# Optimization experiments

Measured on AMD Instinct MI355X. Metric: run time of the kernel, lower is better.

Reference implementation:

```python
import jax, jax.numpy as jnp
import numpy as np

GRID_SIZE = 5
SPLINE_ORDER = 3
GRID_MIN = -1.0
GRID_MAX = 1.0
H = (GRID_MAX - GRID_MIN) / GRID_SIZE          # grid interval
G0 = GRID_MIN - SPLINE_ORDER * H               # first (extended) knot = grid[:,0]


def _basis_matrix():
    # Uniform B-spline power-basis matrix, same recurrence as the torch code.
    M = np.array([[1.0]], dtype=np.float64)
    scalar = 1.0
    for k in range(2, SPLINE_ORDER + 2):
        t1 = np.pad(M, ((0, 1), (0, 0)))
        t3 = np.pad(M, ((1, 0), (0, 0)))
        t2 = np.zeros((k - 1, k))
        t4 = np.zeros((k - 1, k))
        for i in range(k - 1):
            t2[i, i] = i + 1
            t2[i, i + 1] = k - (i + 2)
            t4[i, i] = -1.0
            t4[i, i + 1] = 1.0
        M = t1 @ t2 + t3 @ t4
        scalar *= 1.0 / (k - 1)
    return (M * scalar).astype(np.float32)

BASIS = jnp.asarray(_basis_matrix())  # (spline_order+1, spline_order+1)


def setup_inputs():
    key = jax.random.key(0)
    k1, k2, k3 = jax.random.split(key, 3)
    N, FIN, FOUT = 2048, 128, 128
    x = jax.random.normal(k1, (N, FIN), dtype=jnp.float32)
    base_weight = jax.random.normal(k2, (FOUT, FIN), dtype=jnp.float32) * 0.1
    spline_weight = jax.random.normal(k3, (FIN, FOUT, GRID_SIZE + SPLINE_ORDER), dtype=jnp.float32) * 0.1
    return {"x": x, "base_weight": base_weight, "spline_weight": spline_weight}


def _forward(x, base_weight, spline_weight):
    N, fin = x.shape
    fout = base_weight.shape[0]
    k = SPLINE_ORDER
    # base branch: SiLU activation then linear
    base_out = jax.nn.silu(x) @ base_weight.T                       # (N, fout)
    # input normalization: Hardtanh around grid center (shift=0, scale=1 for [-1,1])
    shift = (GRID_MIN + GRID_MAX) / 2.0
    scale = (GRID_MAX - GRID_MIN) / 2.0
    xn = jnp.clip((x - shift) / scale, -1.0, 1.0) * scale + shift
    # bucketize: bin index + fractional position (replaces floor/compare + torch.nonzero)
    t = (xn - G0) / H
    fl = jnp.floor(t)
    u1 = t - fl                                                     # (x - interval_floor) / interval
    idx = jnp.clip(fl.astype(jnp.int32), k, k + GRID_SIZE - 1)      # clamped knot-interval index
    cfloor = idx - k                                                # (N, fin) first control point index
    # power bases [1, u, u^2, ..., u^k] -> b-spline basis via basis matrix
    pows = u1[..., None] ** jnp.arange(k + 1, dtype=x.dtype)        # (N, fin, k+1)
    bspl = pows @ BASIS.astype(x.dtype)                             # (N, fin, k+1)
    # faithful to torch: spline_weight.view(out, in, -1) memory reinterpretation
    cp = jnp.reshape(spline_weight, (fout, fin, GRID_SIZE + k))
    gidx = cfloor[..., None] + jnp.arange(k + 1)                    # (N, fin, k+1) control point indices
    i_idx = jnp.arange(fin)[None, :, None]
    gathered = cp[:, i_idx, gidx]                                   # (fout, N, fin, k+1)
    gathered = jnp.transpose(gathered, (1, 0, 2, 3))                # (N, fout, fin, k+1)
    # faithful to torch: .view(N, in, k+1, out) memory reinterpretation
    cpr = jnp.reshape(gathered, (N, fin, k + 1, fout))
    # per-feature spline matmul then sum over in_features (KAN aggregation)
    spline_out = jnp.einsum('nij,nijo->no', bspl, cpr)              # (N, fout)
    return base_out + spline_out


def reference(x, base_weight, spline_weight):
    return _forward(x, base_weight, spline_weight)
```

## Files before the change

kernel.cpp:

```cpp
#include <hip/hip_runtime.h>
#include <hip/hip_bf16.h>
#include <math.h>

typedef __attribute__((ext_vector_type(8))) short short8;
typedef __attribute__((ext_vector_type(4))) float floatx4;

static __device__ __forceinline__ unsigned short bfbits(float f) {
    __hip_bfloat16 h = __float2bfloat16(f);
    unsigned short u;
    __builtin_memcpy(&u, &h, 2);
    return u;
}
static __device__ __forceinline__ unsigned pack2(float lo, float hi) {
    return (unsigned)bfbits(lo) | ((unsigned)bfbits(hi) << 16);
}

__global__ __launch_bounds__(256) void kan_prep(
    const float* __restrict__ bw, const float* __restrict__ sw,
    unsigned char* __restrict__ ws)
{
    __shared__ float buf[128 * 65];
    __hip_bfloat16* Bt = (__hip_bfloat16*)ws;
    const int blk = blockIdx.x;
    const int tid = threadIdx.x;

    if (blk < 16) {
        const int a  = tid >> 1;
        const int jh = (tid & 1) * 32;
        const float* src = sw + a * 1024 + blk * 64 + jh;
        float* dst = buf + a * 65 + jh;
#pragma unroll
        for (int i = 0; i < 32; ++i) dst[i] = src[i];
        __syncthreads();
        const int jl = tid >> 2;
        const int aq = (tid & 3) * 32;
        unsigned p[16];
#pragma unroll
        for (int i = 0; i < 16; ++i)
            p[i] = pack2(buf[(aq + 2*i) * 65 + jl], buf[(aq + 2*i + 1) * 65 + jl]);
        uint4* o = (uint4*)(Bt + (blk * 64 + jl) * 128 + aq);
        o[0] = make_uint4(p[0], p[1], p[2], p[3]);
        o[1] = make_uint4(p[4], p[5], p[6], p[7]);
        o[2] = make_uint4(p[8], p[9], p[10], p[11]);
        o[3] = make_uint4(p[12], p[13], p[14], p[15]);
    } else {
        int base = (blk - 16) * 8192 + tid * 32;
        unsigned p[16];
#pragma unroll
        for (int i = 0; i < 8; ++i) {
            float4 v = *(const float4*)(bw + base + i * 4);
            p[2*i]     = pack2(v.x, v.y);
            p[2*i + 1] = pack2(v.z, v.w);
        }
        uint4* o = (uint4*)(Bt + 1024 * 128 + base);
#pragma unroll
        for (int i = 0; i < 4; ++i)
            o[i] = make_uint4(p[4*i], p[4*i+1], p[4*i+2], p[4*i+3]);
    }
}

#define SB_STR 136
#define SP_STR 136
#define ST_STR 68
#define SC_STR 132

__global__ __launch_bounds__(256) void kan_main(
    const float* __restrict__ x,
    const unsigned char* __restrict__ ws,
    float* __restrict__ out)
{
    __shared__ __hip_bfloat16 sP[5 * 16 * SP_STR];
    __shared__ __hip_bfloat16 sB[2][64 * SB_STR];
    __shared__ float sT[2][16 * ST_STR];
    __shared__ unsigned char sC[16 * SC_STR];

    const __hip_bfloat16* Bt = (const __hip_bfloat16*)ws;
    const int tid = threadIdx.x;
    const int nb  = blockIdx.x >> 2;
    const int s   = blockIdx.x & 3;
    const int n0  = nb * 16;

    {
        const int r  = tid >> 4;
        const int i0 = (tid & 15) * 8;
        float v[8];
        *(float4*)(v)     = *(const float4*)(x + (n0 + r) * 128 + i0);
        *(float4*)(v + 4) = *(const float4*)(x + (n0 + r) * 128 + i0 + 4);
        float A5[5][8];
        unsigned char cc8[8];
#pragma unroll
        for (int i = 0; i < 8; ++i) {
            float xv = v[i];
            float si = xv / (1.0f + expf(-xv));
            float xn = fminf(fmaxf(xv, -1.0f), 1.0f);
            float t  = (xn + 2.2f) / 0.4f;
            float u  = t - floorf(t);
            int idx  = (int)floorf(t);
            idx = min(max(idx, 3), 7);
            cc8[i] = (unsigned char)(idx - 3);
            float u2 = u * u, u3 = u2 * u, om = 1.0f - u;
            A5[0][i] = om * om * om * (1.0f / 6.0f);
            A5[1][i] = 0.5f * u3 - u2 + (2.0f / 3.0f);
            A5[2][i] = -0.5f * u3 + 0.5f * u2 + 0.5f * u + (1.0f / 6.0f);
            A5[3][i] = u3 * (1.0f / 6.0f);
            A5[4][i] = si;
        }
#pragma unroll
        for (int g = 0; g < 5; ++g) {
            unsigned p0 = pack2(A5[g][0], A5[g][1]);
            unsigned p1 = pack2(A5[g][2], A5[g][3]);
            unsigned p2 = pack2(A5[g][4], A5[g][5]);
            unsigned p3 = pack2(A5[g][6], A5[g][7]);
            *(uint4*)(sP + (g * 16 + r) * SP_STR + i0) = make_uint4(p0, p1, p2, p3);
        }
        *(unsigned*)(sC + r * SC_STR + i0)     = cc8[0] | (cc8[1]<<8) | (cc8[2]<<16) | (cc8[3]<<24);
        *(unsigned*)(sC + r * SC_STR + i0 + 4) = cc8[4] | (cc8[5]<<8) | (cc8[6]<<16) | (cc8[7]<<24);
    }

    const int w = tid >> 6, l = tid & 63;
    const int m = l & 15, q = l >> 4;
    const int gn  = tid >> 4;
    const int go2 = tid & 15;
    const int br   = tid >> 2;
    const int bseg = (tid & 3) * 32;

    float racc0 = 0.f, racc1 = 0.f;

    uint4 breg[4];
    {
        const uint4* src = (const uint4*)(Bt + (s * 64 + br) * 128 + bseg);
#pragma unroll
        for (int i = 0; i < 4; ++i) breg[i] = src[i];
    }

    for (int t = 0; t < 5; ++t) {
        const int p = t & 1;
        if (t < 4 || tid < 128) {
#pragma unroll
            for (int i = 0; i < 4; ++i)
                *(uint4*)(&sB[p][br * SB_STR + bseg + i * 8]) = breg[i];
        }
        __syncthreads();

        if (t < 3) {
            const uint4* src = (const uint4*)(Bt + ((s + 4*(t+1)) * 64 + br) * 128 + bseg);
#pragma unroll
            for (int i = 0; i < 4; ++i) breg[i] = src[i];
        } else if (t == 3) {
            if (tid < 128) {
                const uint4* src = (const uint4*)(Bt + (1024 + s * 32 + br) * 128 + bseg);
#pragma unroll
                for (int i = 0; i < 4; ++i) breg[i] = src[i];
            }
        }

        if (t > 0) {
            const int tb = t - 1;
            if (tb < 4) {
                int oh  = 8 * s + (go2 >> 1);
                int c   = sC[gn * SC_STR + 32 * tb + oh];
                int rel = 8 * (go2 >> 1) + c + 2 * (go2 & 1);
                racc0 += sT[1 - p][gn * ST_STR + rel];
                racc1 += sT[1 - p][gn * ST_STR + rel + 1];
            }
        }

        if (t < 4 || w < 2) {
            floatx4 acc = {0.f, 0.f, 0.f, 0.f};
#pragma unroll
            for (int kk = 0; kk < 4; ++kk) {
                short8 af  = *(const short8*)(sP + (t * 16 + m) * SP_STR + q * 8 + kk * 32);
                short8 bfr = *(const short8*)(&sB[p][(16 * w + m) * SB_STR + q * 8 + kk * 32]);
                acc = __builtin_amdgcn_mfma_f32_16x16x32_bf16(af, bfr, acc, 0, 0, 0);
            }
#pragma unroll
            for (int r = 0; r < 4; ++r)
                sT[p][(q * 4 + r) * ST_STR + 16 * w + m] = acc[r];
        }
    }
    __syncthreads();
    racc0 += sT[0][gn * ST_STR + 2 * go2];
    racc1 += sT[0][gn * ST_STR + 2 * go2 + 1];

    float2 o2 = make_float2(racc0, racc1);
    *(float2*)(out + (n0 + gn) * 128 + 32 * s + 2 * go2) = o2;
}

extern "C" void kernel_launch(void* const* d_in, const int* in_sizes, int n_in,
                              void* d_out, int out_size, void* d_ws, size_t ws_size,
                              hipStream_t stream) {
    const float* x  = (const float*)d_in[0];
    const float* bw = (const float*)d_in[1];
    const float* sw = (const float*)d_in[2];
    float* out = (float*)d_out;
    unsigned char* ws = (unsigned char*)d_ws;
    kan_prep<<<dim3(18),  dim3(256), 0, stream>>>(bw, sw, ws);
    kan_main<<<dim3(512), dim3(256), 0, stream>>>(x, ws, out);
}
```

Before: 71.26 us.

## Fuse weight prep into main kernel, converting fp32 weights to bf16 per block

Removes the separate prep kernel that transposed and converted spline and base weights to bf16 in a workspace. Each main block now loads fp32 weight slices directly, packs them to bf16 in registers and stores them untransposed in shared memory. The MFMA B fragments are then gathered with strided scalar LDS reads. This saves one kernel launch and the serial dependency between the two kernels, but every block redoes the conversion and reads twice as many weight bytes, and the strided B reads are costlier.

```diff
diff --git a/kernel.cpp b/kernel.cpp
--- a/kernel.cpp
+++ b/kernel.cpp
@@ -15,77 +15,44 @@
     return (unsigned)bfbits(lo) | ((unsigned)bfbits(hi) << 16);
 }
 
-__global__ __launch_bounds__(256) void kan_prep(
-    const float* __restrict__ bw, const float* __restrict__ sw,
-    unsigned char* __restrict__ ws)
-{
-    __shared__ float buf[128 * 65];
-    __hip_bfloat16* Bt = (__hip_bfloat16*)ws;
-    const int blk = blockIdx.x;
-    const int tid = threadIdx.x;
+#define SP_STR  136
+#define SBN_STR 76
+#define SBB_STR 136
+#define ST_STR  68
+#define SC_STR  132
 
-    if (blk < 16) {
-        const int a  = tid >> 1;
-        const int jh = (tid & 1) * 32;
-        const float* src = sw + a * 1024 + blk * 64 + jh;
-        float* dst = buf + a * 65 + jh;
-#pragma unroll
-        for (int i = 0; i < 32; ++i) dst[i] = src[i];
-        __syncthreads();
-        const int jl = tid >> 2;
-        const int aq = (tid & 3) * 32;
-        unsigned p[16];
-#pragma unroll
-        for (int i = 0; i < 16; ++i)
-            p[i] = pack2(buf[(aq + 2*i) * 65 + jl], buf[(aq + 2*i + 1) * 65 + jl]);
-        uint4* o = (uint4*)(Bt + (blk * 64 + jl) * 128 + aq);
-        o[0] = make_uint4(p[0], p[1], p[2], p[3]);
-        o[1] = make_uint4(p[4], p[5], p[6], p[7]);
-        o[2] = make_uint4(p[8], p[9], p[10], p[11]);
-        o[3] = make_uint4(p[12], p[13], p[14], p[15]);
-    } else {
-        int base = (blk - 16) * 8192 + tid * 32;
-        unsigned p[16];
-#pragma unroll
-        for (int i = 0; i < 8; ++i) {
-            float4 v = *(const float4*)(bw + base + i * 4);
-            p[2*i]     = pack2(v.x, v.y);
-            p[2*i + 1] = pack2(v.z, v.w);
-        }
-        uint4* o = (uint4*)(Bt + 1024 * 128 + base);
-#pragma unroll
-        for (int i = 0; i < 4; ++i)
-            o[i] = make_uint4(p[4*i], p[4*i+1], p[4*i+2], p[4*i+3]);
-    }
-}
-
-#define SB_STR 136
-#define SP_STR 136
-#define ST_STR 68
-#define SC_STR 132
-
-__global__ __launch_bounds__(256) void kan_main(
+__global__ __launch_bounds__(256) void kan_fused(
     const float* __restrict__ x,
-    const unsigned char* __restrict__ ws,
+    const float* __restrict__ bw,
+    const float* __restrict__ sw,
     float* __restrict__ out)
 {
-    __shared__ __hip_bfloat16 sP[5 * 16 * SP_STR];
-    __shared__ __hip_bfloat16 sB[2][64 * SB_STR];
+    __shared__ short sP[5 * 16 * SP_STR];
+    __shared__ short sBn[2][128 * SBN_STR];
+    __shared__ short sBb[32 * SBB_STR];
     __shared__ float sT[2][16 * ST_STR];
     __shared__ unsigned char sC[16 * SC_STR];
 
-    const __hip_bfloat16* Bt = (const __hip_bfloat16*)ws;
     const int tid = threadIdx.x;
     const int nb  = blockIdx.x >> 2;
     const int s   = blockIdx.x & 3;
     const int n0  = nb * 16;
 
+    const int ar = tid >> 4;
+    const int sg = tid & 15;
+
+    const int r  = tid >> 4;
+    const int i0 = (tid & 15) * 8;
+    float v[8];
+    *(float4*)(v)     = *(const float4*)(x + (n0 + r) * 128 + i0);
+    *(float4*)(v + 4) = *(const float4*)(x + (n0 + r) * 128 + i0 + 4);
+
+    float4 pre[8];
+#pragma unroll
+    for (int rr = 0; rr < 8; ++rr)
+        pre[rr] = *(const float4*)(sw + (ar + 16 * rr) * 1024 + s * 64 + sg * 4);
+
     {
-        const int r  = tid >> 4;
-        const int i0 = (tid & 15) * 8;
-        float v[8];
-        *(float4*)(v)     = *(const float4*)(x + (n0 + r) * 128 + i0);
-        *(float4*)(v + 4) = *(const float4*)(x + (n0 + r) * 128 + i0 + 4);
         float A5[5][8];
         unsigned char cc8[8];
 #pragma unroll
@@ -111,79 +78,108 @@
             unsigned p1 = pack2(A5[g][2], A5[g][3]);
             unsigned p2 = pack2(A5[g][4], A5[g][5]);
             unsigned p3 = pack2(A5[g][6], A5[g][7]);
-            *(uint4*)(sP + (g * 16 + r) * SP_STR + i0) = make_uint4(p0, p1, p2, p3);
+            *(uint4*)(&sP[(g * 16 + r) * SP_STR + i0]) = make_uint4(p0, p1, p2, p3);
         }
-        *(unsigned*)(sC + r * SC_STR + i0)     = cc8[0] | (cc8[1]<<8) | (cc8[2]<<16) | (cc8[3]<<24);
-        *(unsigned*)(sC + r * SC_STR + i0 + 4) = cc8[4] | (cc8[5]<<8) | (cc8[6]<<16) | (cc8[7]<<24);
+        *(unsigned*)(&sC[r * SC_STR + i0])     = cc8[0] | (cc8[1]<<8) | (cc8[2]<<16) | (cc8[3]<<24);
+        *(unsigned*)(&sC[r * SC_STR + i0 + 4]) = cc8[4] | (cc8[5]<<8) | (cc8[6]<<16) | (cc8[7]<<24);
     }
 
     const int w = tid >> 6, l = tid & 63;
     const int m = l & 15, q = l >> 4;
     const int gn  = tid >> 4;
     const int go2 = tid & 15;
-    const int br   = tid >> 2;
-    const int bseg = (tid & 3) * 32;
+
+    uint2 pk[8];
+#pragma unroll
+    for (int rr = 0; rr < 8; ++rr)
+        pk[rr] = make_uint2(pack2(pre[rr].x, pre[rr].y), pack2(pre[rr].z, pre[rr].w));
 
     float racc0 = 0.f, racc1 = 0.f;
+    float4 bpre[4];
 
-    uint4 breg[4];
-    {
-        const uint4* src = (const uint4*)(Bt + (s * 64 + br) * 128 + bseg);
 #pragma unroll
-        for (int i = 0; i < 4; ++i) breg[i] = src[i];
-    }
-
-    for (int t = 0; t < 5; ++t) {
+    for (int t = 0; t < 4; ++t) {
         const int p = t & 1;
-        if (t < 4 || tid < 128) {
 #pragma unroll
-            for (int i = 0; i < 4; ++i)
-                *(uint4*)(&sB[p][br * SB_STR + bseg + i * 8]) = breg[i];
-        }
+        for (int rr = 0; rr < 8; ++rr)
+            *(uint2*)(&sBn[p][(ar + 16 * rr) * SBN_STR + sg * 4]) = pk[rr];
         __syncthreads();
 
         if (t < 3) {
-            const uint4* src = (const uint4*)(Bt + ((s + 4*(t+1)) * 64 + br) * 128 + bseg);
 #pragma unroll
-            for (int i = 0; i < 4; ++i) breg[i] = src[i];
-        } else if (t == 3) {
-            if (tid < 128) {
-                const uint4* src = (const uint4*)(Bt + (1024 + s * 32 + br) * 128 + bseg);
+            for (int rr = 0; rr < 8; ++rr)
+                pre[rr] = *(const float4*)(sw + (ar + 16 * rr) * 1024 + (s + 4 * (t + 1)) * 64 + sg * 4);
+        } else {
 #pragma unroll
-                for (int i = 0; i < 4; ++i) breg[i] = src[i];
+            for (int i = 0; i < 4; ++i) {
+                int e = i * 256 + tid;
+                bpre[i] = *(const float4*)(bw + (32 * s + (e >> 5)) * 128 + (e & 31) * 4);
             }
         }
 
         if (t > 0) {
-            const int tb = t - 1;
-            if (tb < 4) {
-                int oh  = 8 * s + (go2 >> 1);
-                int c   = sC[gn * SC_STR + 32 * tb + oh];
-                int rel = 8 * (go2 >> 1) + c + 2 * (go2 & 1);
-                racc0 += sT[1 - p][gn * ST_STR + rel];
-                racc1 += sT[1 - p][gn * ST_STR + rel + 1];
-            }
+            int oh  = 8 * s + (go2 >> 1);
+            int c   = sC[gn * SC_STR + 32 * (t - 1) + oh];
+            int rel = 8 * (go2 >> 1) + c + 2 * (go2 & 1);
+            racc0 += sT[1 - p][gn * ST_STR + rel];
+            racc1 += sT[1 - p][gn * ST_STR + rel + 1];
         }
 
-        if (t < 4 || w < 2) {
-            floatx4 acc = {0.f, 0.f, 0.f, 0.f};
+        floatx4 acc = {0.f, 0.f, 0.f, 0.f};
 #pragma unroll
-            for (int kk = 0; kk < 4; ++kk) {
-                short8 af  = *(const short8*)(sP + (t * 16 + m) * SP_STR + q * 8 + kk * 32);
-                short8 bfr = *(const short8*)(&sB[p][(16 * w + m) * SB_STR + q * 8 + kk * 32]);
-                acc = __builtin_amdgcn_mfma_f32_16x16x32_bf16(af, bfr, acc, 0, 0, 0);
-            }
+        for (int kk = 0; kk < 4; ++kk) {
+            short8 af = *(const short8*)(&sP[(t * 16 + m) * SP_STR + q * 8 + kk * 32]);
+            short8 bf;
 #pragma unroll
-            for (int r = 0; r < 4; ++r)
-                sT[p][(q * 4 + r) * ST_STR + 16 * w + m] = acc[r];
+            for (int j2 = 0; j2 < 8; ++j2)
+                bf[j2] = sBn[p][(kk * 32 + q * 8 + j2) * SBN_STR + 16 * w + m];
+            acc = __builtin_amdgcn_mfma_f32_16x16x32_bf16(af, bf, acc, 0, 0, 0);
+        }
+#pragma unroll
+        for (int rr = 0; rr < 4; ++rr)
+            sT[p][(q * 4 + rr) * ST_STR + 16 * w + m] = acc[rr];
+
+        if (t < 3) {
+#pragma unroll
+            for (int rr = 0; rr < 8; ++rr)
+                pk[rr] = make_uint2(pack2(pre[rr].x, pre[rr].y), pack2(pre[rr].z, pre[rr].w));
         }
     }
+
+#pragma unroll
+    for (int i = 0; i < 4; ++i) {
+        int e = i * 256 + tid;
+        *(uint2*)(&sBb[(e >> 5) * SBB_STR + (e & 31) * 4]) =
+            make_uint2(pack2(bpre[i].x, bpre[i].y), pack2(bpre[i].z, bpre[i].w));
+    }
     __syncthreads();
+
+    {
+        int oh  = 8 * s + (go2 >> 1);
+        int c   = sC[gn * SC_STR + 32 * 3 + oh];
+        int rel = 8 * (go2 >> 1) + c + 2 * (go2 & 1);
+        racc0 += sT[1][gn * ST_STR + rel];
+        racc1 += sT[1][gn * ST_STR + rel + 1];
+    }
+
+    if (w < 2) {
+        floatx4 acc = {0.f, 0.f, 0.f, 0.f};
+#pragma unroll
+        for (int kk = 0; kk < 4; ++kk) {
+            short8 af = *(const short8*)(&sP[(4 * 16 + m) * SP_STR + q * 8 + kk * 32]);
+            short8 bf = *(const short8*)(&sBb[(16 * w + m) * SBB_STR + q * 8 + kk * 32]);
+            acc = __builtin_amdgcn_mfma_f32_16x16x32_bf16(af, bf, acc, 0, 0, 0);
+        }
+#pragma unroll
+        for (int rr = 0; rr < 4; ++rr)
+            sT[0][(q * 4 + rr) * ST_STR + 16 * w + m] = acc[rr];
+    }
+    __syncthreads();
+
     racc0 += sT[0][gn * ST_STR + 2 * go2];
     racc1 += sT[0][gn * ST_STR + 2 * go2 + 1];
 
-    float2 o2 = make_float2(racc0, racc1);
-    *(float2*)(out + (n0 + gn) * 128 + 32 * s + 2 * go2) = o2;
+    *(float2*)(out + (n0 + gn) * 128 + 32 * s + 2 * go2) = make_float2(racc0, racc1);
 }
 
 extern "C" void kernel_launch(void* const* d_in, const int* in_sizes, int n_in,
@@ -193,7 +189,5 @@
     const float* bw = (const float*)d_in[1];
     const float* sw = (const float*)d_in[2];
     float* out = (float*)d_out;
-    unsigned char* ws = (unsigned char*)d_ws;
-    kan_prep<<<dim3(18),  dim3(256), 0, stream>>>(bw, sw, ws);
-    kan_main<<<dim3(512), dim3(256), 0, stream>>>(x, ws, out);
+    kan_fused<<<dim3(512), dim3(256), 0, stream>>>(x, bw, sw, out);
 }
```

New measurement: 63.49 us. -10.9%, faster.
